# Performance work log

Measured on AMD Instinct MI355X. Metric: run time of the kernel, lower is better.

The kernel has to match this reference:

```python
import jax, jax.numpy as jnp
import numpy as np

N = 50000        # nodes
E = 800000       # directed edges (before self-loops)
HID = 128
HEADS = 4
LAYERS = 4
D = HID // HEADS  # per-head dim = 32
NEG_SLOPE = 0.2
EPS = 1e-5


def setup_inputs() -> dict:
    key = jax.random.key(0)
    ks = jax.random.split(key, 12)
    s = 0.1
    x = jax.random.normal(ks[0], (N, HID), jnp.float32)
    edge_index = jax.random.randint(ks[1], (2, E), 0, N, jnp.int32)
    # GATv2Conv params per layer: lin_l (source), lin_r (target), att vector, bias
    Wl = s * jax.random.normal(ks[2], (LAYERS, HID, HID), jnp.float32)
    Wr = s * jax.random.normal(ks[3], (LAYERS, HID, HID), jnp.float32)
    att = s * jax.random.normal(ks[4], (LAYERS, HEADS, D), jnp.float32)
    conv_b = jnp.zeros((LAYERS, HID), jnp.float32)
    # GraphNorm params
    gn_w = jnp.ones((LAYERS, HID), jnp.float32)
    gn_b = jnp.zeros((LAYERS, HID), jnp.float32)
    gn_ms = jnp.ones((LAYERS, HID), jnp.float32)  # mean_scale
    # skip projection + final fc
    skip_W = s * jax.random.normal(ks[5], (HID, HID), jnp.float32)
    skip_b = jnp.zeros((HID,), jnp.float32)
    fc_W = s * jax.random.normal(ks[6], (HID, 1), jnp.float32)
    fc_b = jnp.zeros((1,), jnp.float32)
    return {"x": x, "edge_index": edge_index, "Wl": Wl, "Wr": Wr, "att": att,
            "conv_b": conv_b, "gn_w": gn_w, "gn_b": gn_b, "gn_ms": gn_ms,
            "skip_W": skip_W, "skip_b": skip_b, "fc_W": fc_W, "fc_b": fc_b}


def _gatv2_layer(x, src, dst, Wl, Wr, att, bias, n):
    # GATv2Conv: x_l = W_l x_j (messages), x_r = W_r x_i (targets)
    xl = (x @ Wl).reshape(n, HEADS, D)
    xr = (x @ Wr).reshape(n, HEADS, D)
    # edge-wise attention logits: a^T LeakyReLU(x_l[j] + x_r[i])
    e = jax.nn.leaky_relu(xl[src] + xr[dst], NEG_SLOPE)      # [E, H, D]
    score = jnp.einsum('ehd,hd->eh', e, att)                 # [E, H]
    # scatter-softmax over incoming edges of each target node
    smax = jax.ops.segment_max(score, dst, num_segments=n)   # [N, H]
    a = jnp.exp(score - smax[dst])
    denom = jax.ops.segment_sum(a, dst, num_segments=n)
    alpha = a / denom[dst]                                   # [E, H]
    out = jax.ops.segment_sum(alpha[:, :, None] * xl[src], dst, num_segments=n)
    return out.reshape(n, HID) + bias


def _graph_norm(h, w, b, ms):
    # single-graph GraphNorm: x - mean_scale*mean, scaled by per-channel std
    mean = h.mean(axis=0)
    hc = h - ms * mean
    var = (hc * hc).mean(axis=0)
    return w * hc / jnp.sqrt(var + EPS) + b


def reference(x, edge_index, Wl, Wr, att, conv_b, gn_w, gn_b, gn_ms,
              skip_W, skip_b, fc_W, fc_b):
    n = x.shape[0]
    loops = jnp.arange(n, dtype=edge_index.dtype)  # default add_self_loops=True
    src = jnp.concatenate([edge_index[0], loops])
    dst = jnp.concatenate([edge_index[1], loops])
    for l in range(LAYERS):
        h = _gatv2_layer(x, src, dst, Wl[l], Wr[l], att[l], conv_b[l], n)
        h = jax.nn.elu(_graph_norm(h, gn_w[l], gn_b[l], gn_ms[l]))
        x = x + (h @ skip_W + skip_b)  # dropout inactive (eval)
    return (x @ fc_W + fc_b).squeeze(-1)
```

## Files before the change

### kernel.cpp

```cpp
#include <hip/hip_runtime.h>
#include <hip/hip_bf16.h>

#define NN 50000
#define EE 800000
#define NE 850000
#define HID 128
#define NEG_SLOPE 0.2f
#define EPSN 1e-5f
#define NB 196
#define BCAP 6144
#define TB 4096
#define REP 128
#define NPB 8
#define GCAP 512
#define LOG2E 1.4426950408889634f

typedef __attribute__((ext_vector_type(8))) short bf16x8;
typedef __attribute__((ext_vector_type(4))) float f32x4;
typedef __attribute__((ext_vector_type(2))) float f32x2;

__device__ __forceinline__ unsigned short f2b(float f) {
    unsigned u = __float_as_uint(f);
    unsigned r = (u + 0x7FFFu + ((u >> 16) & 1u)) >> 16;
    return (unsigned short)r;
}
__device__ __forceinline__ float b2f(unsigned short u) {
    return __uint_as_float(((unsigned)u) << 16);
}
__device__ __forceinline__ float2 up2(unsigned u) {
    return make_float2(__uint_as_float(u << 16),
                       __uint_as_float(u & 0xFFFF0000u));
}
__device__ __forceinline__ f32x2 up2p(unsigned u) {
    f32x2 r;
    r[0] = __uint_as_float(u << 16);
    r[1] = __uint_as_float(u & 0xFFFF0000u);
    return r;
}
__device__ __forceinline__ f32x2 pka(f32x2 a, f32x2 b) {
    f32x2 d;
    asm("v_pk_add_f32 %0, %1, %2" : "=v"(d) : "v"(a), "v"(b));
    return d;
}
__device__ __forceinline__ f32x2 pkm(f32x2 a, f32x2 b) {
    f32x2 d;
    asm("v_pk_mul_f32 %0, %1, %2" : "=v"(d) : "v"(a), "v"(b));
    return d;
}
__device__ __forceinline__ f32x2 pkf(f32x2 a, f32x2 b, f32x2 c) {
    f32x2 d;
    asm("v_pk_fma_f32 %0, %1, %2, %3" : "=v"(d) : "v"(a), "v"(b), "v"(c));
    return d;
}
__device__ __forceinline__ f32x2 pabs2(f32x2 v) {
    f32x2 r;
    r[0] = __builtin_fabsf(v[0]);
    r[1] = __builtin_fabsf(v[1]);
    return r;
}
#define QPADD(p, CTRL)                                                         \
    __int_as_float(__builtin_amdgcn_update_dpp(                                \
        __float_as_int(p), __float_as_int(p), CTRL, 0xF, 0xF, false))


__global__ void k_prep(const float* __restrict__ x, const float* __restrict__ Wl,
                       const float* __restrict__ Wr, const float* __restrict__ skip_W,
                       unsigned short* __restrict__ xb, unsigned short* __restrict__ wt,
                       unsigned short* __restrict__ st, int* __restrict__ bcnt,
                       float* __restrict__ stats) {
    int i = blockIdx.x * blockDim.x + threadIdx.x;
    if (i < NN * HID / 4) {
        float4 v = *(const float4*)&x[i * 4];
        ushort4 o = {f2b(v.x), f2b(v.y), f2b(v.z), f2b(v.w)};
        *(ushort4*)&xb[i * 4] = o;
    }
    if (i < NB) bcnt[i] = 0;
    if (i < REP * 256) stats[i] = 0.f;
    if (i < 4 * 256 * 128) {
        int l = i >> 15, idx = i & 32767;
        int j = idx & 7;
        int l16 = (idx >> 3) & 15;
        int quad = (idx >> 7) & 3;
        int ks = (idx >> 9) & 3;
        int ct = idx >> 11;
        int c = ct * 16 + l16;
        int k = quad * 8 + ks * 32 + j;
        float v = (c < 128) ? Wl[l * 16384 + k * 128 + c]
                            : Wr[l * 16384 + k * 128 + (c - 128)];
        wt[i] = f2b(v);
    } else if (i < 4 * 256 * 128 + 128 * 128) {
        int idx = i - 4 * 256 * 128;
        int j = idx & 7;
        int l16 = (idx >> 3) & 15;
        int quad = (idx >> 7) & 3;
        int ks = (idx >> 9) & 3;
        int ct = idx >> 11;
        int c = ct * 16 + l16;
        int k = quad * 8 + ks * 32 + j;
        st[idx] = f2b(skip_W[k * 128 + c]);
    }
}

__global__ void __launch_bounds__(256) k_bin(const int* __restrict__ ei,
                                             int* __restrict__ bcnt,
                                             unsigned* __restrict__ bbuf) {
    __shared__ int hist[NB];
    __shared__ int gbase[NB];
    int t = threadIdx.x;
    for (int b = t; b < NB; b += 256) hist[b] = 0;
    __syncthreads();
    int e0 = blockIdx.x * TB;
    unsigned ent[16];
    int bkt[16];
#pragma unroll
    for (int k = 0; k < 16; k++) {
        int e = e0 + k * 256 + t;
        if (e < NE) {
            int src, dst;
            if (e < EE) { src = ei[e]; dst = ei[EE + e]; }
            else        { src = e - EE; dst = src; }
            int b = dst >> 8;
            ent[k] = ((unsigned)(dst & 255) << 17) | (unsigned)src;
            bkt[k] = b;
            atomicAdd(&hist[b], 1);
        } else bkt[k] = -1;
    }
    __syncthreads();
    for (int b = t; b < NB; b += 256) {
        int c = hist[b];
        gbase[b] = (c > 0) ? atomicAdd(&bcnt[b], c) : 0;
        hist[b] = 0;
    }
    __syncthreads();
#pragma unroll
    for (int k = 0; k < 16; k++) {
        int b = bkt[k];
        if (b >= 0) {
            int pos = gbase[b] + atomicAdd(&hist[b], 1);
            if (pos < BCAP) bbuf[(size_t)b * BCAP + pos] = ent[k];
        }
    }
}

__global__ void __launch_bounds__(256) k_bucket_csr(
    const unsigned* __restrict__ bbuf, const int* __restrict__ bcnt,
    int* __restrict__ row_ptr, int* __restrict__ csr_off) {
    __shared__ unsigned se[BCAP];
    __shared__ int pre[256];
    __shared__ int hist[256], scn[256], exs[256], cur[256];
    int b = blockIdx.x, t = threadIdx.x;
    int bv = (t < NB) ? bcnt[t] : 0;
    pre[t] = bv;
    __syncthreads();
    for (int o = 1; o < 256; o <<= 1) {
        int u = (t >= o) ? pre[t - o] : 0;
        __syncthreads();
        pre[t] += u;
        __syncthreads();
    }
    int cntb = bcnt[b];
    int base = pre[b] - cntb;
    int cnt = min(cntb, BCAP);
    hist[t] = 0;
    cur[t] = 0;
    __syncthreads();
    for (int j = t; j < cnt; j += 256) {
        unsigned e = bbuf[(size_t)b * BCAP + j];
        se[j] = e;
        atomicAdd(&hist[e >> 17], 1);
    }
    __syncthreads();
    int v = hist[t];
    scn[t] = v;
    __syncthreads();
    for (int o = 1; o < 256; o <<= 1) {
        int u = (t >= o) ? scn[t - o] : 0;
        __syncthreads();
        scn[t] += u;
        __syncthreads();
    }
    int ex = scn[t] - v;
    exs[t] = ex;
    int node = b * 256 + t;
    if (node < NN) row_ptr[node] = base + ex;
    if (b == NB - 1 && t == 0) row_ptr[NN] = NE;
    __syncthreads();
    for (int j = t; j < cnt; j += 256) {
        unsigned e = se[j];
        int dl = e >> 17;
        int p = exs[dl] + atomicAdd(&cur[dl], 1);
        csr_off[base + p] = (int)((e & 0x1FFFFu) << 9);
    }
}

__global__ void __launch_bounds__(256) k_gemm_dual_mfma(
    const unsigned short* __restrict__ Xb, const unsigned short* __restrict__ WT,
    unsigned short* __restrict__ C) {
    int w = threadIdx.x >> 6, lane = threadIdx.x & 63;
    int quad = lane >> 4, l16 = lane & 15;
    int r0 = blockIdx.x * 64 + w * 16;
    int lrow = r0 + l16; if (lrow >= NN) lrow = NN - 1;
    const unsigned short* arow = Xb + (size_t)lrow * 128 + quad * 8;
    bf16x8 a[4];
#pragma unroll
    for (int ks = 0; ks < 4; ks++) a[ks] = *(const bf16x8*)(arow + ks * 32);
    const unsigned short* wbase = WT + quad * 128 + l16 * 8;
    f32x4 acc[16];
#pragma unroll
    for (int ct = 0; ct < 16; ct++) acc[ct] = (f32x4){0, 0, 0, 0};
#pragma unroll
    for (int ct = 0; ct < 16; ct++) {
#pragma unroll
        for (int ks = 0; ks < 4; ks++) {
            bf16x8 b = *(const bf16x8*)(wbase + ct * 2048 + ks * 512);
            acc[ct] = __builtin_amdgcn_mfma_f32_16x16x32_bf16(a[ks], b, acc[ct], 0, 0, 0);
        }
    }
    int sr = r0 + quad * 4;
#pragma unroll
    for (int ct = 0; ct < 16; ct++) {
#pragma unroll
        for (int r = 0; r < 4; r++) {
            int rr = sr + r;
            if (rr < NN) C[(size_t)rr * 256 + ct * 16 + l16] = f2b(acc[ct][r]);
        }
    }
}

__global__ void __launch_bounds__(1024) k_finalize(
    float* __restrict__ stats, const float* __restrict__ gn_w,
    const float* __restrict__ gn_b, const float* __restrict__ gn_ms,
    float* __restrict__ scoff) {
    __shared__ float red[1024];
    __shared__ float tot[256];
    int t = threadIdx.x;
    int col = t & 255, part = t >> 8;
    float s = 0.f;
    for (int r = part * (REP / 4); r < (part + 1) * (REP / 4); r++)
        s += stats[(size_t)r * 256 + col];
    red[t] = s;
    __syncthreads();
    if (part == 0) tot[col] = red[col] + red[col + 256] + red[col + 512] + red[col + 768];
    __syncthreads();
    for (int j = t; j < REP * 256; j += 1024) stats[j] = 0.f;
    if (t < 128) {
        const float invN = 1.0f / (float)NN;
        float mean = tot[t] * invN;
        float ex2 = tot[128 + t] * invN;
        float ms = gn_ms[t];
        float var = ex2 - (2.f * ms - ms * ms) * mean * mean;
        float wsc = gn_w[t] * rsqrtf(var + EPSN);
        scoff[t] = wsc;
        scoff[128 + t] = gn_b[t] - wsc * ms * mean;
    }
}

__device__ __forceinline__ void skip_core(
    const unsigned short* __restrict__ hbufb, const float* __restrict__ scoff,
    const unsigned short* __restrict__ ST, int lrow, int quad, int l16,
    f32x4 (&acc)[8]) {
    const unsigned short* hrow = hbufb + (size_t)lrow * 128 + quad * 8;
    const unsigned short* stbase = ST + quad * 128 + l16 * 8;
#pragma unroll
    for (int ct = 0; ct < 8; ct++) acc[ct] = (f32x4){0, 0, 0, 0};
#pragma unroll
    for (int ks = 0; ks < 4; ks++) {
        int k0 = ks * 32;
        int kc = quad * 8 + k0;
        uint4 hw = *(const uint4*)(hrow + k0);
        float2 h01 = up2(hw.x), h23 = up2(hw.y), h45 = up2(hw.z), h67 = up2(hw.w);
        float4 sc0 = *(const float4*)(scoff + kc);
        float4 sc1 = *(const float4*)(scoff + kc + 4);
        float4 of0 = *(const float4*)(scoff + 128 + kc);
        float4 of1 = *(const float4*)(scoff + 128 + kc + 4);
        float e[8];
        e[0] = fmaf(sc0.x, h01.x, of0.x); e[1] = fmaf(sc0.y, h01.y, of0.y);
        e[2] = fmaf(sc0.z, h23.x, of0.z); e[3] = fmaf(sc0.w, h23.y, of0.w);
        e[4] = fmaf(sc1.x, h45.x, of1.x); e[5] = fmaf(sc1.y, h45.y, of1.y);
        e[6] = fmaf(sc1.z, h67.x, of1.z); e[7] = fmaf(sc1.w, h67.y, of1.w);
        bf16x8 af;
#pragma unroll
        for (int j = 0; j < 8; j++) {
            float v = e[j];
            v = (v > 0.f) ? v : (__expf(v) - 1.f);
            af[j] = (short)f2b(v);
        }
#pragma unroll
        for (int ct = 0; ct < 8; ct++) {
            bf16x8 b = *(const bf16x8*)(stbase + ct * 2048 + ks * 512);
            acc[ct] = __builtin_amdgcn_mfma_f32_16x16x32_bf16(af, b, acc[ct], 0, 0, 0);
        }
    }
}

__global__ void __launch_bounds__(256) k_skip_dual(
    const unsigned short* __restrict__ hbufb, const float* __restrict__ scoff,
    const unsigned short* __restrict__ ST, const float* __restrict__ skip_b,
    unsigned short* __restrict__ Xb16,
    const unsigned short* __restrict__ WTnext, unsigned short* __restrict__ xlr) {
    __shared__ unsigned short tileX[64][136];
    __shared__ unsigned short tileC[4][16][264];
    int t = threadIdx.x;
    int w = t >> 6, lane = t & 63;
    int quad = lane >> 4, l16 = lane & 15;
    int r0b = blockIdx.x * 64;
    int r0 = r0b + w * 16;
    int lrow = r0 + l16; if (lrow >= NN) lrow = NN - 1;
#pragma unroll
    for (int it = 0; it < 4; it++) {
        int idx = it * 256 + t;
        int row = idx >> 4;
        int c8 = (idx & 15) * 8;
        int rr = r0b + row;
        uint4 v = (rr < NN) ? *(const uint4*)&Xb16[(size_t)rr * 128 + c8]
                            : (uint4){0, 0, 0, 0};
        *(uint4*)&tileX[row][c8] = v;
    }
    f32x4 acc[8];
    skip_core(hbufb, scoff, ST, lrow, quad, l16, acc);
    __syncthreads();
#pragma unroll
    for (int ct = 0; ct < 8; ct++) {
        int c = ct * 16 + l16;
        float sb = skip_b[c];
#pragma unroll
        for (int r = 0; r < 4; r++) {
            int wrow = w * 16 + quad * 4 + r;
            float v = b2f(tileX[wrow][c]) + acc[ct][r] + sb;
            tileX[wrow][c] = f2b(v);
        }
    }
    __syncthreads();
#pragma unroll
    for (int it = 0; it < 4; it++) {
        int idx = it * 256 + t;
        int row = idx >> 4;
        int c8 = (idx & 15) * 8;
        int rr = r0b + row;
        if (rr < NN) *(uint4*)&Xb16[(size_t)rr * 128 + c8] = *(const uint4*)&tileX[row][c8];
    }
    int wrowA = w * 16 + l16;
    bf16x8 a[4];
#pragma unroll
    for (int ks = 0; ks < 4; ks++)
        a[ks] = *(const bf16x8*)&tileX[wrowA][quad * 8 + ks * 32];
    const unsigned short* wbase = WTnext + quad * 128 + l16 * 8;
    f32x4 dacc[16];
#pragma unroll
    for (int ct = 0; ct < 16; ct++) dacc[ct] = (f32x4){0, 0, 0, 0};
#pragma unroll
    for (int ct = 0; ct < 16; ct++) {
#pragma unroll
        for (int ks = 0; ks < 4; ks++) {
            bf16x8 b = *(const bf16x8*)(wbase + ct * 2048 + ks * 512);
            dacc[ct] = __builtin_amdgcn_mfma_f32_16x16x32_bf16(a[ks], b, dacc[ct], 0, 0, 0);
        }
    }
#pragma unroll
    for (int ct = 0; ct < 16; ct++) {
#pragma unroll
        for (int r = 0; r < 4; r++)
            tileC[w][quad * 4 + r][ct * 16 + l16] = f2b(dacc[ct][r]);
    }
    __syncthreads();
#pragma unroll
    for (int it = 0; it < 8; it++) {
        int idx = it * 64 + lane;
        int row = idx >> 5;
        int c8 = (idx & 31) * 8;
        int rr = r0 + row;
        if (rr < NN) *(uint4*)&xlr[(size_t)rr * 256 + c8] = *(const uint4*)&tileC[w][row][c8];
    }
}

__global__ void __launch_bounds__(256) k_skip_fc(
    const unsigned short* __restrict__ hbufb, const float* __restrict__ scoff,
    const unsigned short* __restrict__ ST, const float* __restrict__ skip_b,
    const unsigned short* __restrict__ Xb16,
    const float* __restrict__ fc_W, const float* __restrict__ fc_b,
    float* __restrict__ out) {
    __shared__ unsigned short tileX[64][136];
    int t = threadIdx.x;
    int w = t >> 6, lane = t & 63;
    int quad = lane >> 4, l16 = lane & 15;
    int r0b = blockIdx.x * 64;
    int r0 = r0b + w * 16;
    int lrow = r0 + l16; if (lrow >= NN) lrow = NN - 1;
#pragma unroll
    for (int it = 0; it < 4; it++) {
        int idx = it * 256 + t;
        int row = idx >> 4;
        int c8 = (idx & 15) * 8;
        int rr = r0b + row;
        uint4 v = (rr < NN) ? *(const uint4*)&Xb16[(size_t)rr * 128 + c8]
                            : (uint4){0, 0, 0, 0};
        *(uint4*)&tileX[row][c8] = v;
    }
    f32x4 acc[8];
    skip_core(hbufb, scoff, ST, lrow, quad, l16, acc);
    __syncthreads();
    float p[4] = {0.f, 0.f, 0.f, 0.f};
#pragma unroll
    for (int ct = 0; ct < 8; ct++) {
        int c = ct * 16 + l16;
        float sb = skip_b[c];
        float fw = fc_W[c];
#pragma unroll
        for (int r = 0; r < 4; r++) {
            int wrow = w * 16 + quad * 4 + r;
            float v = b2f(tileX[wrow][c]) + acc[ct][r] + sb;
            p[r] = fmaf(v, fw, p[r]);
        }
    }
#pragma unroll
    for (int r = 0; r < 4; r++) {
        p[r] += __shfl_xor(p[r], 1);
        p[r] += __shfl_xor(p[r], 2);
        p[r] += __shfl_xor(p[r], 4);
        p[r] += __shfl_xor(p[r], 8);
    }
    if (l16 == 0) {
        float fb = fc_b[0];
#pragma unroll
        for (int r = 0; r < 4; r++) {
            int rr = r0 + quad * 4 + r;
            if (rr < NN) out[rr] = p[r] + fb;
        }
    }
}

__global__ void __launch_bounds__(128) k_gat_node(
    const unsigned short* __restrict__ xlr,
    const float* __restrict__ att, const float* __restrict__ conv_b,
    const int* __restrict__ row_ptr, const int* __restrict__ csr_off,
    unsigned short* __restrict__ houtb, float* __restrict__ stats) {
    __shared__ int s_off[GCAP];
    int t = threadIdx.x;
    int wv = t >> 6, lane = t & 63;
    int g = lane >> 4;
    int l = lane & 15;
    int i0 = blockIdx.x * NPB;
    int e0 = row_ptr[i0];
    int cnt = row_ptr[i0 + NPB] - e0;
    int stged = min(cnt, GCAP);
    for (int k = t; k < stged; k += 128) s_off[k] = csr_off[e0 + k];
    int n0 = i0 + wv * 4;
    int rp[5];
#pragma unroll
    for (int k = 0; k <= 4; k++) rp[k] = row_ptr[n0 + k];
    __syncthreads();

    const char* xbytes = (const char*)xlr;
    int lofs = 16 * l;
    f32x2 at06[4], at04[4];
    {
        float4 a0 = *(const float4*)&att[8 * l];
        float4 a1 = *(const float4*)&att[8 * l + 4];
        const float c6 = 0.6f * LOG2E, c4 = 0.4f * LOG2E;
        at06[0][0] = a0.x * c6; at06[0][1] = a0.y * c6;
        at06[1][0] = a0.z * c6; at06[1][1] = a0.w * c6;
        at06[2][0] = a1.x * c6; at06[2][1] = a1.y * c6;
        at06[3][0] = a1.z * c6; at06[3][1] = a1.w * c6;
        at04[0][0] = a0.x * c4; at04[0][1] = a0.y * c4;
        at04[1][0] = a0.z * c4; at04[1][1] = a0.w * c4;
        at04[2][0] = a1.x * c4; at04[2][1] = a1.y * c4;
        at04[3][0] = a1.z * c4; at04[3][1] = a1.w * c4;
    }
    int c0p = 8 * l + 2 * g;
    float2 cbp = *(const float2*)&conv_b[c0p];
    float saA = 0.f, sqA = 0.f, saB = 0.f, sqB = 0.f;

    uint4 xr_raw = *(const uint4*)(xbytes + (size_t)n0 * 512 + 256 + lofs);
    int start = rp[0] - e0, end = rp[1] - e0;
    int j = start + g;
    bool v0 = j < end;
    bool v1 = (j + 4) < end;
    int o0 = 0, o1 = 0;
    if (v0) o0 = (j < stged) ? s_off[j] : csr_off[e0 + j];
    if (v1) o1 = (j + 4 < stged) ? s_off[j + 4] : csr_off[e0 + j + 4];
    uint4 xw0 = {0, 0, 0, 0}, xw1 = {0, 0, 0, 0};
    if (v0) xw0 = *(const uint4*)(xbytes + (size_t)(unsigned)o0 + lofs);
    if (v1) xw1 = *(const uint4*)(xbytes + (size_t)(unsigned)o1 + lofs);

    for (int nn = 0; nn < 4; nn++) {
        f32x2 xr2[4];
        xr2[0] = up2p(xr_raw.x); xr2[1] = up2p(xr_raw.y);
        xr2[2] = up2p(xr_raw.z); xr2[3] = up2p(xr_raw.w);
        float den = 0.f;
        f32x2 acc[4];
#pragma unroll
        for (int k = 0; k < 4; k++) { acc[k][0] = 0.f; acc[k][1] = 0.f; }
        while (v0) {
            bool v2 = (j + 8) < end;
            int o2 = 0;
            if (v2) o2 = (j + 8 < stged) ? s_off[j + 8] : csr_off[e0 + j + 8];
            uint4 xw2 = {0, 0, 0, 0};
            if (v2) xw2 = *(const uint4*)(xbytes + (size_t)(unsigned)o2 + lofs);
            f32x2 f0 = up2p(xw0.x), f1 = up2p(xw0.y);
            f32x2 f2v = up2p(xw0.z), f3 = up2p(xw0.w);
            f32x2 s0 = pka(f0, xr2[0]);
            f32x2 s1 = pka(f1, xr2[1]);
            f32x2 s2 = pka(f2v, xr2[2]);
            f32x2 s3 = pka(f3, xr2[3]);
            f32x2 ps = pkm(at06[0], s0);
            ps = pkf(at04[0], pabs2(s0), ps);
            ps = pkf(at06[1], s1, ps);
            ps = pkf(at04[1], pabs2(s1), ps);
            ps = pkf(at06[2], s2, ps);
            ps = pkf(at04[2], pabs2(s2), ps);
            ps = pkf(at06[3], s3, ps);
            ps = pkf(at04[3], pabs2(s3), ps);
            float p = ps[0] + ps[1];
            p += QPADD(p, 0xB1);
            p += QPADD(p, 0x4E);
            float w = exp2f(p);
            den += w;
            f32x2 w2; w2[0] = w; w2[1] = w;
            acc[0] = pkf(w2, f0, acc[0]);
            acc[1] = pkf(w2, f1, acc[1]);
            acc[2] = pkf(w2, f2v, acc[2]);
            acc[3] = pkf(w2, f3, acc[3]);
            j += 4;
            v0 = v1; v1 = v2;
            xw0 = xw1; xw1 = xw2;
        }
        float r0v = acc[0][0], r1v = acc[0][1], r2v = acc[1][0], r3v = acc[1][1];
        float r4v = acc[2][0], r5v = acc[2][1], r6v = acc[3][0], r7v = acc[3][1];
        float dn = den;
        if (nn < 3) {
            xr_raw = *(const uint4*)(xbytes + (size_t)(n0 + nn + 1) * 512 + 256 + lofs);
            start = rp[nn + 1] - e0; end = rp[nn + 2] - e0;
            j = start + g;
            v0 = j < end;
            v1 = (j + 4) < end;
            o0 = 0; o1 = 0;
            if (v0) o0 = (j < stged) ? s_off[j] : csr_off[e0 + j];
            if (v1) o1 = (j + 4 < stged) ? s_off[j + 4] : csr_off[e0 + j + 4];
            xw0 = (uint4){0, 0, 0, 0}; xw1 = (uint4){0, 0, 0, 0};
            if (v0) xw0 = *(const uint4*)(xbytes + (size_t)(unsigned)o0 + lofs);
            if (v1) xw1 = *(const uint4*)(xbytes + (size_t)(unsigned)o1 + lofs);
        }
        r0v += __shfl_xor(r0v, 16); r0v += __shfl_xor(r0v, 32);
        r1v += __shfl_xor(r1v, 16); r1v += __shfl_xor(r1v, 32);
        r2v += __shfl_xor(r2v, 16); r2v += __shfl_xor(r2v, 32);
        r3v += __shfl_xor(r3v, 16); r3v += __shfl_xor(r3v, 32);
        r4v += __shfl_xor(r4v, 16); r4v += __shfl_xor(r4v, 32);
        r5v += __shfl_xor(r5v, 16); r5v += __shfl_xor(r5v, 32);
        r6v += __shfl_xor(r6v, 16); r6v += __shfl_xor(r6v, 32);
        r7v += __shfl_xor(r7v, 16); r7v += __shfl_xor(r7v, 32);
        dn  += __shfl_xor(dn, 16);  dn  += __shfl_xor(dn, 32);
        float rA = (g == 0) ? r0v : (g == 1) ? r2v : (g == 2) ? r4v : r6v;
        float rB = (g == 0) ? r1v : (g == 1) ? r3v : (g == 2) ? r5v : r7v;
        float invd = 1.0f / dn;
        float hA = fmaf(rA, invd, cbp.x);
        float hB = fmaf(rB, invd, cbp.y);
        unsigned pkv = (unsigned)f2b(hA) | ((unsigned)f2b(hB) << 16);
        *(unsigned*)&houtb[(size_t)(n0 + nn) * 128 + c0p] = pkv;
        saA += hA; sqA += hA * hA;
        saB += hB; sqB += hB * hB;
    }
    {
        float* srep = stats + (size_t)(blockIdx.x & (REP - 1)) * 256;
        atomicAdd(&srep[c0p], saA);
        atomicAdd(&srep[c0p + 1], saB);
        atomicAdd(&srep[128 + c0p], sqA);
        atomicAdd(&srep[128 + c0p + 1], sqB);
    }
}

extern "C" void kernel_launch(void* const* d_in, const int* in_sizes, int n_in,
                              void* d_out, int out_size, void* d_ws, size_t ws_size,
                              hipStream_t stream) {
    const float* x_in   = (const float*)d_in[0];
    const int*   ei     = (const int*)d_in[1];
    const float* Wl     = (const float*)d_in[2];
    const float* Wr     = (const float*)d_in[3];
    const float* att    = (const float*)d_in[4];
    const float* conv_b = (const float*)d_in[5];
    const float* gn_w   = (const float*)d_in[6];
    const float* gn_b   = (const float*)d_in[7];
    const float* gn_ms  = (const float*)d_in[8];
    const float* skip_W = (const float*)d_in[9];
    const float* skip_b = (const float*)d_in[10];
    const float* fc_W   = (const float*)d_in[11];
    const float* fc_b   = (const float*)d_in[12];
    float* out = (float*)d_out;

    float* ws = (float*)d_ws;
    float* stats = ws;
    float* scoff = stats + REP * 256;
    unsigned short* xlr   = (unsigned short*)(scoff + 256);
    unsigned short* b16X  = xlr + (size_t)NN * 256;
    unsigned short* hbufb = b16X + NN * HID;
    unsigned short* wt    = hbufb + NN * HID;
    unsigned short* st    = wt + 4 * 256 * 128;
    int* row_ptr = (int*)(st + 128 * 128);
    int* bcnt    = row_ptr + NN + 1;
    int* csr_off = bcnt + NB;
    unsigned* bbuf = (unsigned*)(csr_off + NE);

    k_prep<<<(NN * HID / 4 + 255) / 256, 256, 0, stream>>>(
        x_in, Wl, Wr, skip_W, b16X, wt, st, bcnt, stats);

    k_bin<<<(NE + TB - 1) / TB, 256, 0, stream>>>(ei, bcnt, bbuf);
    k_bucket_csr<<<NB, 256, 0, stream>>>(bbuf, bcnt, row_ptr, csr_off);

    const int rtiles = (NN + 63) / 64;
    const int gat_blocks = (NN + NPB - 1) / NPB;
    k_gemm_dual_mfma<<<rtiles, 256, 0, stream>>>(b16X, wt, xlr);
    for (int l = 0; l < 4; l++) {
        k_gat_node<<<gat_blocks, 128, 0, stream>>>(
            xlr, att + l * HID, conv_b + l * HID, row_ptr, csr_off,
            hbufb, stats);
        k_finalize<<<1, 1024, 0, stream>>>(stats, gn_w + l * HID,
                                           gn_b + l * HID, gn_ms + l * HID, scoff);
        if (l < 3) {
            k_skip_dual<<<rtiles, 256, 0, stream>>>(
                hbufb, scoff, st, skip_b, b16X,
                wt + (size_t)(l + 1) * 256 * 128, xlr);
        } else {
            k_skip_fc<<<rtiles, 256, 0, stream>>>(
                hbufb, scoff, st, skip_b, b16X, fc_W, fc_b, out);
        }
    }
}
```

Measured before the change: 441.0 us.

## Fuse GraphNorm finalize into skip kernels, deepen edge prefetch, widen GAT blocks

Drops the single-block k_finalize launch per layer. Each skip kernel block now reduces the per-layer stats replicas into shared-memory scale and offset values, with REP cut to 32 and separate stats buffers per layer so no zeroing pass is needed. The GAT node kernel now handles 16 nodes per 256-thread block and uses a three-deep rotating prefetch of source features, with split partial sums in the score reduction. The trade is redundant stats reduction in every skip block and more atomic contention on fewer replicas. It also assumes NN is divisible by NPB.

```diff
diff --git a/kernel.cpp b/kernel.cpp
--- a/kernel.cpp
+++ b/kernel.cpp
@@ -10,9 +10,9 @@
 #define NB 196
 #define BCAP 6144
 #define TB 4096
-#define REP 128
-#define NPB 8
-#define GCAP 512
+#define REP 32
+#define NPB 16
+#define GCAP 768
 #define LOG2E 1.4426950408889634f
 
 typedef __attribute__((ext_vector_type(8))) short bf16x8;
@@ -75,7 +75,7 @@
         *(ushort4*)&xb[i * 4] = o;
     }
     if (i < NB) bcnt[i] = 0;
-    if (i < REP * 256) stats[i] = 0.f;
+    if (i < 4 * REP * 256) stats[i] = 0.f;
     if (i < 4 * 256 * 128) {
         int l = i >> 15, idx = i & 32767;
         int j = idx & 7;
@@ -227,36 +227,31 @@
     }
 }
 
-__global__ void __launch_bounds__(1024) k_finalize(
-    float* __restrict__ stats, const float* __restrict__ gn_w,
+__device__ __forceinline__ void scoff_reduce(
+    const float* __restrict__ stats_l, const float* __restrict__ gn_w,
     const float* __restrict__ gn_b, const float* __restrict__ gn_ms,
-    float* __restrict__ scoff) {
-    __shared__ float red[1024];
-    __shared__ float tot[256];
-    int t = threadIdx.x;
-    int col = t & 255, part = t >> 8;
-    float s = 0.f;
-    for (int r = part * (REP / 4); r < (part + 1) * (REP / 4); r++)
-        s += stats[(size_t)r * 256 + col];
-    red[t] = s;
-    __syncthreads();
-    if (part == 0) tot[col] = red[col] + red[col + 256] + red[col + 512] + red[col + 768];
-    __syncthreads();
-    for (int j = t; j < REP * 256; j += 1024) stats[j] = 0.f;
+    int t, float* s_tot, float* s_sc) {
+    float ssum = 0.f;
+    const float* sp = stats_l + t;
+#pragma unroll
+    for (int r = 0; r < REP; r++) ssum += sp[r * 256];
+    s_tot[t] = ssum;
+    __syncthreads();
     if (t < 128) {
         const float invN = 1.0f / (float)NN;
-        float mean = tot[t] * invN;
-        float ex2 = tot[128 + t] * invN;
+        float mean = s_tot[t] * invN;
+        float ex2 = s_tot[128 + t] * invN;
         float ms = gn_ms[t];
         float var = ex2 - (2.f * ms - ms * ms) * mean * mean;
         float wsc = gn_w[t] * rsqrtf(var + EPSN);
-        scoff[t] = wsc;
-        scoff[128 + t] = gn_b[t] - wsc * ms * mean;
-    }
+        s_sc[t] = wsc;
+        s_sc[128 + t] = gn_b[t] - wsc * ms * mean;
+    }
+    __syncthreads();
 }
 
 __device__ __forceinline__ void skip_core(
-    const unsigned short* __restrict__ hbufb, const float* __restrict__ scoff,
+    const unsigned short* __restrict__ hbufb, const float* scoff,
     const unsigned short* __restrict__ ST, int lrow, int quad, int l16,
     f32x4 (&acc)[8]) {
     const unsigned short* hrow = hbufb + (size_t)lrow * 128 + quad * 8;
@@ -294,12 +289,16 @@
 }
 
 __global__ void __launch_bounds__(256) k_skip_dual(
-    const unsigned short* __restrict__ hbufb, const float* __restrict__ scoff,
+    const unsigned short* __restrict__ hbufb, const float* __restrict__ stats_l,
+    const float* __restrict__ gn_w, const float* __restrict__ gn_b,
+    const float* __restrict__ gn_ms,
     const unsigned short* __restrict__ ST, const float* __restrict__ skip_b,
     unsigned short* __restrict__ Xb16,
     const unsigned short* __restrict__ WTnext, unsigned short* __restrict__ xlr) {
     __shared__ unsigned short tileX[64][136];
     __shared__ unsigned short tileC[4][16][264];
+    __shared__ __align__(16) float s_tot[256];
+    __shared__ __align__(16) float s_sc[256];
     int t = threadIdx.x;
     int w = t >> 6, lane = t & 63;
     int quad = lane >> 4, l16 = lane & 15;
@@ -316,8 +315,9 @@
                             : (uint4){0, 0, 0, 0};
         *(uint4*)&tileX[row][c8] = v;
     }
+    scoff_reduce(stats_l, gn_w, gn_b, gn_ms, t, s_tot, s_sc);
     f32x4 acc[8];
-    skip_core(hbufb, scoff, ST, lrow, quad, l16, acc);
+    skip_core(hbufb, s_sc, ST, lrow, quad, l16, acc);
     __syncthreads();
 #pragma unroll
     for (int ct = 0; ct < 8; ct++) {
@@ -374,12 +374,16 @@
 }
 
 __global__ void __launch_bounds__(256) k_skip_fc(
-    const unsigned short* __restrict__ hbufb, const float* __restrict__ scoff,
+    const unsigned short* __restrict__ hbufb, const float* __restrict__ stats_l,
+    const float* __restrict__ gn_w, const float* __restrict__ gn_b,
+    const float* __restrict__ gn_ms,
     const unsigned short* __restrict__ ST, const float* __restrict__ skip_b,
     const unsigned short* __restrict__ Xb16,
     const float* __restrict__ fc_W, const float* __restrict__ fc_b,
     float* __restrict__ out) {
     __shared__ unsigned short tileX[64][136];
+    __shared__ __align__(16) float s_tot[256];
+    __shared__ __align__(16) float s_sc[256];
     int t = threadIdx.x;
     int w = t >> 6, lane = t & 63;
     int quad = lane >> 4, l16 = lane & 15;
@@ -396,8 +400,9 @@
                             : (uint4){0, 0, 0, 0};
         *(uint4*)&tileX[row][c8] = v;
     }
+    scoff_reduce(stats_l, gn_w, gn_b, gn_ms, t, s_tot, s_sc);
     f32x4 acc[8];
-    skip_core(hbufb, scoff, ST, lrow, quad, l16, acc);
+    skip_core(hbufb, s_sc, ST, lrow, quad, l16, acc);
     __syncthreads();
     float p[4] = {0.f, 0.f, 0.f, 0.f};
 #pragma unroll
@@ -429,11 +434,40 @@
     }
 }
 
-__global__ void __launch_bounds__(128) k_gat_node(
+__device__ __forceinline__ void proc_edge(
+    const uint4& xw, const f32x2* xr2, const f32x2* at06, const f32x2* at04,
+    float& den, f32x2* acc) {
+    f32x2 f0 = up2p(xw.x), f1 = up2p(xw.y);
+    f32x2 f2v = up2p(xw.z), f3 = up2p(xw.w);
+    f32x2 s0 = pka(f0, xr2[0]);
+    f32x2 s1 = pka(f1, xr2[1]);
+    f32x2 s2 = pka(f2v, xr2[2]);
+    f32x2 s3 = pka(f3, xr2[3]);
+    f32x2 ps1 = pkm(at06[0], s0);
+    ps1 = pkf(at04[0], pabs2(s0), ps1);
+    ps1 = pkf(at06[1], s1, ps1);
+    ps1 = pkf(at04[1], pabs2(s1), ps1);
+    f32x2 ps2 = pkm(at06[2], s2);
+    ps2 = pkf(at04[2], pabs2(s2), ps2);
+    ps2 = pkf(at06[3], s3, ps2);
+    ps2 = pkf(at04[3], pabs2(s3), ps2);
+    float p = (ps1[0] + ps2[0]) + (ps1[1] + ps2[1]);
+    p += QPADD(p, 0xB1);
+    p += QPADD(p, 0x4E);
+    float w = exp2f(p);
+    den += w;
+    f32x2 w2; w2[0] = w; w2[1] = w;
+    acc[0] = pkf(w2, f0, acc[0]);
+    acc[1] = pkf(w2, f1, acc[1]);
+    acc[2] = pkf(w2, f2v, acc[2]);
+    acc[3] = pkf(w2, f3, acc[3]);
+}
+
+__global__ void __launch_bounds__(256) k_gat_node(
     const unsigned short* __restrict__ xlr,
     const float* __restrict__ att, const float* __restrict__ conv_b,
     const int* __restrict__ row_ptr, const int* __restrict__ csr_off,
-    unsigned short* __restrict__ houtb, float* __restrict__ stats) {
+    unsigned short* __restrict__ houtb, float* __restrict__ stats_l) {
     __shared__ int s_off[GCAP];
     int t = threadIdx.x;
     int wv = t >> 6, lane = t & 63;
@@ -443,7 +477,7 @@
     int e0 = row_ptr[i0];
     int cnt = row_ptr[i0 + NPB] - e0;
     int stged = min(cnt, GCAP);
-    for (int k = t; k < stged; k += 128) s_off[k] = csr_off[e0 + k];
+    for (int k = t; k < stged; k += 256) s_off[k] = csr_off[e0 + k];
     int n0 = i0 + wv * 4;
     int rp[5];
 #pragma unroll
@@ -473,14 +507,14 @@
     uint4 xr_raw = *(const uint4*)(xbytes + (size_t)n0 * 512 + 256 + lofs);
     int start = rp[0] - e0, end = rp[1] - e0;
     int j = start + g;
-    bool v0 = j < end;
-    bool v1 = (j + 4) < end;
-    int o0 = 0, o1 = 0;
-    if (v0) o0 = (j < stged) ? s_off[j] : csr_off[e0 + j];
-    if (v1) o1 = (j + 4 < stged) ? s_off[j + 4] : csr_off[e0 + j + 4];
-    uint4 xw0 = {0, 0, 0, 0}, xw1 = {0, 0, 0, 0};
-    if (v0) xw0 = *(const uint4*)(xbytes + (size_t)(unsigned)o0 + lofs);
-    if (v1) xw1 = *(const uint4*)(xbytes + (size_t)(unsigned)o1 + lofs);
+    bool vA = j < end;
+    bool vB = (j + 4) < end;
+    bool vC = false;
+    uint4 xwA = {0, 0, 0, 0}, xwB = {0, 0, 0, 0}, xwC = {0, 0, 0, 0};
+    if (vA) { int o = (j < stged) ? s_off[j] : csr_off[e0 + j];
+              xwA = *(const uint4*)(xbytes + (size_t)(unsigned)o + lofs); }
+    if (vB) { int o = (j + 4 < stged) ? s_off[j + 4] : csr_off[e0 + j + 4];
+              xwB = *(const uint4*)(xbytes + (size_t)(unsigned)o + lofs); }
 
     for (int nn = 0; nn < 4; nn++) {
         f32x2 xr2[4];
@@ -490,39 +524,34 @@
         f32x2 acc[4];
 #pragma unroll
         for (int k = 0; k < 4; k++) { acc[k][0] = 0.f; acc[k][1] = 0.f; }
-        while (v0) {
-            bool v2 = (j + 8) < end;
-            int o2 = 0;
-            if (v2) o2 = (j + 8 < stged) ? s_off[j + 8] : csr_off[e0 + j + 8];
-            uint4 xw2 = {0, 0, 0, 0};
-            if (v2) xw2 = *(const uint4*)(xbytes + (size_t)(unsigned)o2 + lofs);
-            f32x2 f0 = up2p(xw0.x), f1 = up2p(xw0.y);
-            f32x2 f2v = up2p(xw0.z), f3 = up2p(xw0.w);
-            f32x2 s0 = pka(f0, xr2[0]);
-            f32x2 s1 = pka(f1, xr2[1]);
-            f32x2 s2 = pka(f2v, xr2[2]);
-            f32x2 s3 = pka(f3, xr2[3]);
-            f32x2 ps = pkm(at06[0], s0);
-            ps = pkf(at04[0], pabs2(s0), ps);
-            ps = pkf(at06[1], s1, ps);
-            ps = pkf(at04[1], pabs2(s1), ps);
-            ps = pkf(at06[2], s2, ps);
-            ps = pkf(at04[2], pabs2(s2), ps);
-            ps = pkf(at06[3], s3, ps);
-            ps = pkf(at04[3], pabs2(s3), ps);
-            float p = ps[0] + ps[1];
-            p += QPADD(p, 0xB1);
-            p += QPADD(p, 0x4E);
-            float w = exp2f(p);
-            den += w;
-            f32x2 w2; w2[0] = w; w2[1] = w;
-            acc[0] = pkf(w2, f0, acc[0]);
-            acc[1] = pkf(w2, f1, acc[1]);
-            acc[2] = pkf(w2, f2v, acc[2]);
-            acc[3] = pkf(w2, f3, acc[3]);
-            j += 4;
-            v0 = v1; v1 = v2;
-            xw0 = xw1; xw1 = xw2;
+        for (;;) {
+            if (!vA) break;
+            {
+                bool vn = (j + 8) < end;
+                if (vn) { int o = (j + 8 < stged) ? s_off[j + 8] : csr_off[e0 + j + 8];
+                          xwC = *(const uint4*)(xbytes + (size_t)(unsigned)o + lofs); }
+                vC = vn;
+                proc_edge(xwA, xr2, at06, at04, den, acc);
+                j += 4;
+            }
+            if (!vB) break;
+            {
+                bool vn = (j + 8) < end;
+                if (vn) { int o = (j + 8 < stged) ? s_off[j + 8] : csr_off[e0 + j + 8];
+                          xwA = *(const uint4*)(xbytes + (size_t)(unsigned)o + lofs); }
+                vA = vn;
+                proc_edge(xwB, xr2, at06, at04, den, acc);
+                j += 4;
+            }
+            if (!vC) break;
+            {
+                bool vn = (j + 8) < end;
+                if (vn) { int o = (j + 8 < stged) ? s_off[j + 8] : csr_off[e0 + j + 8];
+                          xwB = *(const uint4*)(xbytes + (size_t)(unsigned)o + lofs); }
+                vB = vn;
+                proc_edge(xwC, xr2, at06, at04, den, acc);
+                j += 4;
+            }
         }
         float r0v = acc[0][0], r1v = acc[0][1], r2v = acc[1][0], r3v = acc[1][1];
         float r4v = acc[2][0], r5v = acc[2][1], r6v = acc[3][0], r7v = acc[3][1];
@@ -531,14 +560,13 @@
             xr_raw = *(const uint4*)(xbytes + (size_t)(n0 + nn + 1) * 512 + 256 + lofs);
             start = rp[nn + 1] - e0; end = rp[nn + 2] - e0;
             j = start + g;
-            v0 = j < end;
-            v1 = (j + 4) < end;
-            o0 = 0; o1 = 0;
-            if (v0) o0 = (j < stged) ? s_off[j] : csr_off[e0 + j];
-            if (v1) o1 = (j + 4 < stged) ? s_off[j + 4] : csr_off[e0 + j + 4];
-            xw0 = (uint4){0, 0, 0, 0}; xw1 = (uint4){0, 0, 0, 0};
-            if (v0) xw0 = *(const uint4*)(xbytes + (size_t)(unsigned)o0 + lofs);
-            if (v1) xw1 = *(const uint4*)(xbytes + (size_t)(unsigned)o1 + lofs);
+            vA = j < end;
+            vB = (j + 4) < end;
+            xwA = (uint4){0, 0, 0, 0}; xwB = (uint4){0, 0, 0, 0};
+            if (vA) { int o = (j < stged) ? s_off[j] : csr_off[e0 + j];
+                      xwA = *(const uint4*)(xbytes + (size_t)(unsigned)o + lofs); }
+            if (vB) { int o = (j + 4 < stged) ? s_off[j + 4] : csr_off[e0 + j + 4];
+                      xwB = *(const uint4*)(xbytes + (size_t)(unsigned)o + lofs); }
         }
         r0v += __shfl_xor(r0v, 16); r0v += __shfl_xor(r0v, 32);
         r1v += __shfl_xor(r1v, 16); r1v += __shfl_xor(r1v, 32);
@@ -560,7 +588,7 @@
         saB += hB; sqB += hB * hB;
     }
     {
-        float* srep = stats + (size_t)(blockIdx.x & (REP - 1)) * 256;
+        float* srep = stats_l + (size_t)(blockIdx.x & (REP - 1)) * 256;
         atomicAdd(&srep[c0p], saA);
         atomicAdd(&srep[c0p + 1], saB);
         atomicAdd(&srep[128 + c0p], sqA);
@@ -588,8 +616,7 @@
 
     float* ws = (float*)d_ws;
     float* stats = ws;
-    float* scoff = stats + REP * 256;
-    unsigned short* xlr   = (unsigned short*)(scoff + 256);
+    unsigned short* xlr   = (unsigned short*)(stats + 4 * REP * 256);
     unsigned short* b16X  = xlr + (size_t)NN * 256;
     unsigned short* hbufb = b16X + NN * HID;
     unsigned short* wt    = hbufb + NN * HID;
@@ -606,21 +633,21 @@
     k_bucket_csr<<<NB, 256, 0, stream>>>(bbuf, bcnt, row_ptr, csr_off);
 
     const int rtiles = (NN + 63) / 64;
-    const int gat_blocks = (NN + NPB - 1) / NPB;
+    const int gat_blocks = NN / NPB;
     k_gemm_dual_mfma<<<rtiles, 256, 0, stream>>>(b16X, wt, xlr);
     for (int l = 0; l < 4; l++) {
-        k_gat_node<<<gat_blocks, 128, 0, stream>>>(
+        float* stats_l = stats + (size_t)l * REP * 256;
+        k_gat_node<<<gat_blocks, 256, 0, stream>>>(
             xlr, att + l * HID, conv_b + l * HID, row_ptr, csr_off,
-            hbufb, stats);
-        k_finalize<<<1, 1024, 0, stream>>>(stats, gn_w + l * HID,
-                                           gn_b + l * HID, gn_ms + l * HID, scoff);
+            hbufb, stats_l);
         if (l < 3) {
             k_skip_dual<<<rtiles, 256, 0, stream>>>(
-                hbufb, scoff, st, skip_b, b16X,
-                wt + (size_t)(l + 1) * 256 * 128, xlr);
+                hbufb, stats_l, gn_w + l * HID, gn_b + l * HID, gn_ms + l * HID,
+                st, skip_b, b16X, wt + (size_t)(l + 1) * 256 * 128, xlr);
         } else {
             k_skip_fc<<<rtiles, 256, 0, stream>>>(
-                hbufb, scoff, st, skip_b, b16X, fc_W, fc_b, out);
-        }
-    }
-}
+                hbufb, stats_l, gn_w + l * HID, gn_b + l * HID, gn_ms + l * HID,
+                st, skip_b, b16X, fc_W, fc_b, out);
+        }
+    }
+}
```

After: 467.0 us. 5.9% more time.
